# Kernel tuning notes

Measured on AMD Instinct MI355X. Metric: run time of the kernel, lower is better.

The kernel has to match this reference:

```python
import jax, jax.numpy as jnp
import numpy as np

D_MODEL = 768
N_HEAD = 12
HEAD_DIM = D_MODEL // N_HEAD
D_FF = 4 * D_MODEL
EPS = 1e-5


def setup_inputs() -> dict:
    key = jax.random.key(0)
    ks = jax.random.split(key, 12)
    B, S = 4, 1024
    s = 0.02
    return {
        "x": jax.random.normal(ks[0], (B, S, D_MODEL), jnp.float32),
        "ln1_g": jnp.ones((D_MODEL,), jnp.float32),
        "ln1_b": jnp.zeros((D_MODEL,), jnp.float32),
        "ln2_g": jnp.ones((D_MODEL,), jnp.float32),
        "ln2_b": jnp.zeros((D_MODEL,), jnp.float32),
        "w_attn": jax.random.normal(ks[1], (D_MODEL, 3 * D_MODEL), jnp.float32) * s,
        "b_attn": jnp.zeros((3 * D_MODEL,), jnp.float32),
        "w_proj": jax.random.normal(ks[2], (D_MODEL, D_MODEL), jnp.float32) * s,
        "b_proj": jnp.zeros((D_MODEL,), jnp.float32),
        "w_fc": jax.random.normal(ks[3], (D_MODEL, D_FF), jnp.float32) * s,
        "b_fc": jnp.zeros((D_FF,), jnp.float32),
        "w_mlp_proj": jax.random.normal(ks[4], (D_FF, D_MODEL), jnp.float32) * s,
        "b_mlp_proj": jnpp.zeros((D_MODEL,), jnp.float32) if False else jnp.zeros((D_MODEL,), jnp.float32),
    }


def layer_norm(x, g, b):
    mu = jnp.mean(x, axis=-1, keepdims=True)
    var = jnp.mean(jnp.square(x - mu), axis=-1, keepdims=True)
    return (x - mu) * jax.lax.rsqrt(var + EPS) * g + b


def attention(x, w_attn, b_attn, w_proj, b_proj):
    B, S, _ = x.shape
    qkv = x @ w_attn + b_attn                      # [B,S,3D]
    q, k, v = jnp.split(qkv, 3, axis=-1)
    def heads(t):
        return t.reshape(B, S, N_HEAD, HEAD_DIM).transpose(0, 2, 1, 3)  # [B,H,S,hd]
    q, k, v = heads(q), heads(k), heads(v)
    scale = HEAD_DIM ** (-0.5)
    att = jnp.einsum("bhqd,bhkd->bhqk", q, k) * scale
    # additive causal mask: strictly-upper triangle gets -1e9 (matches TF source)
    mask = 1.0 - jnp.tril(jnp.ones((S, S), att.dtype))
    att = att + mask * (-1e9)
    att = jax.nn.softmax(att, axis=-1)
    y = jnp.einsum("bhqk,bhkd->bhqd", att, v)
    y = y.transpose(0, 2, 1, 3).reshape(B, S, D_MODEL)
    return y @ w_proj + b_proj


def mlp(x, w_fc, b_fc, w_mlp_proj, b_mlp_proj):
    h = jax.nn.gelu(x @ w_fc + b_fc, approximate=True)
    return h @ w_mlp_proj + b_mlp_proj


def reference(x, ln1_g, ln1_b, ln2_g, ln2_b, w_attn, b_attn, w_proj, b_proj,
              w_fc, b_fc, w_mlp_proj, b_mlp_proj):
    x = x + attention(layer_norm(x, ln1_g, ln1_b), w_attn, b_attn, w_proj, b_proj)
    x = x + mlp(layer_norm(x, ln2_g, ln2_b), w_fc, b_fc, w_mlp_proj, b_mlp_proj)
    return x
```

## Files before the change

kernel.cpp:

```cpp
#include <hip/hip_runtime.h>

typedef unsigned short u16;
typedef short bf8_t __attribute__((ext_vector_type(8)));
typedef float f32x4 __attribute__((ext_vector_type(4)));

__device__ __forceinline__ u16 f2bf(float f) {
  unsigned u = __builtin_bit_cast(unsigned, f);
  unsigned r = (u + 0x7fffu + ((u >> 16) & 1u)) >> 16;
  return (u16)r;
}

__device__ __forceinline__ void gld16(const void* g, void* l) {
  __builtin_amdgcn_global_load_lds((const __attribute__((address_space(1))) unsigned int*)g,
                                   (__attribute__((address_space(3))) unsigned int*)l, 16, 0, 0);
}

#define MFMA(a, b, c) __builtin_amdgcn_mfma_f32_16x16x32_bf16((a), (b), (c), 0, 0, 0)

__global__ void wtrans_kernel(const float* __restrict__ W, u16* __restrict__ WT, int K, int N) {
  __shared__ float tile[32][33];
  const int n0 = blockIdx.x << 5, k0 = blockIdx.y << 5;
  const int tx = threadIdx.x, ty = threadIdx.y;
#pragma unroll
  for (int i = 0; i < 4; i++) {
    const int r = ty + (i << 3);
    tile[r][tx] = W[(size_t)(k0 + r) * N + n0 + tx];
  }
  __syncthreads();
#pragma unroll
  for (int i = 0; i < 4; i++) {
    const int r = ty + (i << 3);
    WT[(size_t)(n0 + r) * K + k0 + tx] = f2bf(tile[tx][r]);
  }
}

__global__ void ln_kernel(const float* __restrict__ x, const float* __restrict__ g,
                          const float* __restrict__ bb, u16* __restrict__ o) {
  const int row = blockIdx.x, t = threadIdx.x;
  const float* xr = x + (size_t)row * 768;
  float v[3];
#pragma unroll
  for (int i = 0; i < 3; i++) v[i] = xr[t + (i << 8)];
  float s = v[0] + v[1] + v[2];
#pragma unroll
  for (int off = 1; off < 64; off <<= 1) s += __shfl_xor(s, off, 64);
  __shared__ float red[4];
  const int w = t >> 6;
  if ((t & 63) == 0) red[w] = s;
  __syncthreads();
  const float mu = (red[0] + red[1] + red[2] + red[3]) * (1.f / 768.f);
  float q = 0.f;
#pragma unroll
  for (int i = 0; i < 3; i++) {
    v[i] -= mu;
    q += v[i] * v[i];
  }
#pragma unroll
  for (int off = 1; off < 64; off <<= 1) q += __shfl_xor(q, off, 64);
  __syncthreads();
  if ((t & 63) == 0) red[w] = q;
  __syncthreads();
  const float var = (red[0] + red[1] + red[2] + red[3]) * (1.f / 768.f);
  const float rs = rsqrtf(var + 1e-5f);
#pragma unroll
  for (int i = 0; i < 3; i++) {
    const int idx = t + (i << 8);
    o[(size_t)row * 768 + idx] = f2bf(v[i] * rs * g[idx] + bb[idx]);
  }
}

template <int EPI>
__global__ void gemm_kernel(const u16* __restrict__ A, const u16* __restrict__ BT,
                            const float* __restrict__ bias, const float* __restrict__ res,
                            void* __restrict__ outp, int M, int N, int K) {
  __shared__ __align__(16) u16 As[128 * 32];
  __shared__ __align__(16) u16 Bs[128 * 32];
  const int m0 = blockIdx.y << 7, n0 = blockIdx.x << 7;
  const int tid = threadIdx.x, lane = tid & 63, w = tid >> 6;
  const int wr = w >> 1, wc = w & 1;
  const int l16 = lane & 15, kg = lane >> 4;
  f32x4 acc[4][4];
  const f32x4 fz = {0.f, 0.f, 0.f, 0.f};
#pragma unroll
  for (int i = 0; i < 4; i++)
#pragma unroll
    for (int j = 0; j < 4; j++) acc[i][j] = fz;

  const int c1 = (w << 6) + lane;
  const int r1 = c1 >> 2, ko1 = (c1 & 3) << 3;
  const int c2 = c1 + 256;
  const int r2 = c2 >> 2, ko2 = (c2 & 3) << 3;
  const int nkt = K >> 5;
  for (int kt = 0; kt < nkt; kt++) {
    const int k0 = kt << 5;
    __syncthreads();
    gld16(A + (size_t)(m0 + r1) * K + k0 + ko1, As + (size_t)(c1 - lane) * 8);
    gld16(A + (size_t)(m0 + r2) * K + k0 + ko2, As + (size_t)(c2 - lane) * 8);
    gld16(BT + (size_t)(n0 + r1) * K + k0 + ko1, Bs + (size_t)(c1 - lane) * 8);
    gld16(BT + (size_t)(n0 + r2) * K + k0 + ko2, Bs + (size_t)(c2 - lane) * 8);
    __syncthreads();
    bf8_t af[4], bfr[4];
#pragma unroll
    for (int mf = 0; mf < 4; mf++)
      af[mf] = *(const bf8_t*)&As[((wr << 6) + (mf << 4) + l16) * 32 + (kg << 3)];
#pragma unroll
    for (int nf = 0; nf < 4; nf++)
      bfr[nf] = *(const bf8_t*)&Bs[((wc << 6) + (nf << 4) + l16) * 32 + (kg << 3)];
#pragma unroll
    for (int mf = 0; mf < 4; mf++)
#pragma unroll
      for (int nf = 0; nf < 4; nf++) acc[mf][nf] = MFMA(af[mf], bfr[nf], acc[mf][nf]);
  }
#pragma unroll
  for (int mf = 0; mf < 4; mf++) {
#pragma unroll
    for (int nf = 0; nf < 4; nf++) {
      const int col = n0 + (wc << 6) + (nf << 4) + l16;
      const float bv = bias[col];
#pragma unroll
      for (int j = 0; j < 4; j++) {
        const int row = m0 + (wr << 6) + (mf << 4) + (kg << 2) + j;
        float v = acc[mf][nf][j] + bv;
        if constexpr (EPI == 0) {
          ((u16*)outp)[(size_t)row * N + col] = f2bf(v);
        } else if constexpr (EPI == 1) {
          const float u = 0.7978845608f * (v + 0.044715f * v * v * v);
          const float e = __expf(2.f * u);
          const float th = 1.f - 2.f / (e + 1.f);
          ((u16*)outp)[(size_t)row * N + col] = f2bf(0.5f * v * (1.f + th));
        } else {
          v += res[(size_t)row * N + col];
          ((float*)outp)[(size_t)row * N + col] = v;
        }
      }
    }
  }
}

__global__ void attn_kernel(const u16* __restrict__ qkv, u16* __restrict__ y) {
  __shared__ __align__(16) u16 Qs[64 * 64];
  __shared__ __align__(16) u16 Ks[64 * 64];
  __shared__ __align__(16) u16 Vt[64 * 72];
  __shared__ __align__(16) u16 Ps[4][16 * 72];
  const int qt = blockIdx.x, bh = blockIdx.y;
  const int b = bh / 12, h = bh - b * 12;
  const size_t brow = (size_t)b << 10;
  const int q0 = qt << 6;
  const int tid = threadIdx.x, lane = tid & 63, w = tid >> 6;
  const int l16 = lane & 15, kg = lane >> 4;

  const int c1 = (w << 6) + lane, c2 = c1 + 256;
  const int row1 = c1 >> 3, cc1 = c1 & 7;
  const int row2 = c2 >> 3, cc2 = c2 & 7;
  const int sw1 = ((cc1 ^ (row1 & 7)) << 3);
  const int sw2 = ((cc2 ^ (row2 & 7)) << 3);

  {
    const int cb = h << 6;
    gld16(qkv + (brow + q0 + row1) * 2304 + cb + sw1, Qs + (size_t)(c1 - lane) * 8);
    gld16(qkv + (brow + q0 + row2) * 2304 + cb + sw2, Qs + (size_t)(c2 - lane) * 8);
  }
  __syncthreads();
  bf8_t qf[2];
  {
    const int qrow = (w << 4) + l16;
#pragma unroll
    for (int hd = 0; hd < 2; hd++) {
      const int ch = (kg + (hd << 2)) ^ (qrow & 7);
      qf[hd] = *(const bf8_t*)&Qs[qrow * 64 + (ch << 3)];
    }
  }

  f32x4 oacc[4];
  const f32x4 fz = {0.f, 0.f, 0.f, 0.f};
#pragma unroll
  for (int dg = 0; dg < 4; dg++) oacc[dg] = fz;
  float mrun[4], lrun[4];
#pragma unroll
  for (int j = 0; j < 4; j++) {
    mrun[j] = -1e30f;
    lrun[j] = 0.f;
  }

  for (int kt = 0; kt <= qt; kt++) {
    __syncthreads();
    {
      const int cb = 768 + (h << 6);
      gld16(qkv + (brow + (kt << 6) + row1) * 2304 + cb + sw1, Ks + (size_t)(c1 - lane) * 8);
      gld16(qkv + (brow + (kt << 6) + row2) * 2304 + cb + sw2, Ks + (size_t)(c2 - lane) * 8);
    }
    {
      const int cb = 1536 + (h << 6);
#pragma unroll
      for (int ii = 0; ii < 2; ii++) {
        const int c = tid + (ii << 8);
        const int key = c >> 3, d0 = (c & 7) << 3;
        const bf8_t vv = *(const bf8_t*)(qkv + (brow + (kt << 6) + key) * 2304 + cb + d0);
#pragma unroll
        for (int i = 0; i < 8; i++) Vt[(d0 + i) * 72 + key] = (u16)vv[i];
      }
    }
    __syncthreads();
    float sv[4][4];
#pragma unroll
    for (int g = 0; g < 4; g++) {
      f32x4 z = fz;
      const int key = (g << 4) + l16;
#pragma unroll
      for (int hd = 0; hd < 2; hd++) {
        const int ch = (kg + (hd << 2)) ^ (key & 7);
        const bf8_t kf = *(const bf8_t*)&Ks[key * 64 + (ch << 3)];
        z = MFMA(qf[hd], kf, z);
      }
      const int gkey = (kt << 6) + key;
#pragma unroll
      for (int j = 0; j < 4; j++) {
        const int grow = q0 + (w << 4) + (kg << 2) + j;
        sv[g][j] = (gkey <= grow) ? z[j] * 0.125f : -1e30f;
      }
    }
    float tm[4];
#pragma unroll
    for (int j = 0; j < 4; j++)
      tm[j] = fmaxf(fmaxf(sv[0][j], sv[1][j]), fmaxf(sv[2][j], sv[3][j]));
#pragma unroll
    for (int o = 1; o < 16; o <<= 1)
#pragma unroll
      for (int j = 0; j < 4; j++) tm[j] = fmaxf(tm[j], __shfl_xor(tm[j], o, 64));
    float corr[4], tsum[4];
#pragma unroll
    for (int j = 0; j < 4; j++) {
      const float mn = fmaxf(mrun[j], tm[j]);
      corr[j] = __expf(mrun[j] - mn);
      mrun[j] = mn;
      tsum[j] = 0.f;
    }
#pragma unroll
    for (int g = 0; g < 4; g++)
#pragma unroll
      for (int j = 0; j < 4; j++) {
        const float p = __expf(sv[g][j] - mrun[j]);
        sv[g][j] = p;
        tsum[j] += p;
      }
#pragma unroll
    for (int o = 1; o < 16; o <<= 1)
#pragma unroll
      for (int j = 0; j < 4; j++) tsum[j] += __shfl_xor(tsum[j], o, 64);
#pragma unroll
    for (int j = 0; j < 4; j++) lrun[j] = lrun[j] * corr[j] + tsum[j];
#pragma unroll
    for (int dg = 0; dg < 4; dg++)
#pragma unroll
      for (int j = 0; j < 4; j++) oacc[dg][j] *= corr[j];
#pragma unroll
    for (int g = 0; g < 4; g++)
#pragma unroll
      for (int j = 0; j < 4; j++)
        Ps[w][((kg << 2) + j) * 72 + (g << 4) + l16] = f2bf(sv[g][j]);
    bf8_t pf[2];
#pragma unroll
    for (int kh = 0; kh < 2; kh++)
      pf[kh] = *(const bf8_t*)&Ps[w][l16 * 72 + (kg << 3) + (kh << 5)];
#pragma unroll
    for (int dg = 0; dg < 4; dg++)
#pragma unroll
      for (int kh = 0; kh < 2; kh++) {
        const bf8_t vf = *(const bf8_t*)&Vt[((dg << 4) + l16) * 72 + (kg << 3) + (kh << 5)];
        oacc[dg] = MFMA(pf[kh], vf, oacc[dg]);
      }
  }
  float inv[4];
#pragma unroll
  for (int j = 0; j < 4; j++) inv[j] = 1.f / lrun[j];
#pragma unroll
  for (int dg = 0; dg < 4; dg++)
#pragma unroll
    for (int j = 0; j < 4; j++) {
      const size_t grow = brow + q0 + (w << 4) + (kg << 2) + j;
      y[grow * 768 + (h << 6) + (dg << 4) + l16] = f2bf(oacc[dg][j] * inv[j]);
    }
}

extern "C" void kernel_launch(void* const* d_in, const int* in_sizes, int n_in,
                              void* d_out, int out_size, void* d_ws, size_t ws_size,
                              hipStream_t stream) {
  const float* x = (const float*)d_in[0];
  const float* ln1_g = (const float*)d_in[1];
  const float* ln1_b = (const float*)d_in[2];
  const float* ln2_g = (const float*)d_in[3];
  const float* ln2_b = (const float*)d_in[4];
  const float* w_attn = (const float*)d_in[5];
  const float* b_attn = (const float*)d_in[6];
  const float* w_proj = (const float*)d_in[7];
  const float* b_proj = (const float*)d_in[8];
  const float* w_fc = (const float*)d_in[9];
  const float* b_fc = (const float*)d_in[10];
  const float* w_mlp = (const float*)d_in[11];
  const float* b_mlp = (const float*)d_in[12];
  float* out = (float*)d_out;

  char* ws = (char*)d_ws;
  u16* wqkvT = (u16*)(ws + 0);
  u16* wprojT = (u16*)(ws + 3538944);
  u16* wfcT = (u16*)(ws + 4718592);
  u16* wmlpT = (u16*)(ws + 9437184);
  u16* xn = (u16*)(ws + 14155776);
  u16* qkv = (u16*)(ws + 20447232);
  u16* hbuf = (u16*)(ws + 20447232);
  u16* yb = (u16*)(ws + 45613056);
  float* x1 = (float*)(ws + 51904512);

  const dim3 wtb(32, 8);
  wtrans_kernel<<<dim3(2304 / 32, 768 / 32), wtb, 0, stream>>>(w_attn, wqkvT, 768, 2304);
  wtrans_kernel<<<dim3(768 / 32, 768 / 32), wtb, 0, stream>>>(w_proj, wprojT, 768, 768);
  wtrans_kernel<<<dim3(3072 / 32, 768 / 32), wtb, 0, stream>>>(w_fc, wfcT, 768, 3072);
  wtrans_kernel<<<dim3(768 / 32, 3072 / 32), wtb, 0, stream>>>(w_mlp, wmlpT, 3072, 768);

  ln_kernel<<<4096, 256, 0, stream>>>(x, ln1_g, ln1_b, xn);
  gemm_kernel<0><<<dim3(2304 / 128, 4096 / 128), 256, 0, stream>>>(xn, wqkvT, b_attn, nullptr,
                                                                   qkv, 4096, 2304, 768);
  attn_kernel<<<dim3(16, 48), 256, 0, stream>>>(qkv, yb);
  gemm_kernel<2><<<dim3(768 / 128, 4096 / 128), 256, 0, stream>>>(yb, wprojT, b_proj, x, x1,
                                                                  4096, 768, 768);
  ln_kernel<<<4096, 256, 0, stream>>>(x1, ln2_g, ln2_b, xn);
  gemm_kernel<1><<<dim3(3072 / 128, 4096 / 128), 256, 0, stream>>>(xn, wfcT, b_fc, nullptr,
                                                                   hbuf, 4096, 3072, 768);
  gemm_kernel<2><<<dim3(768 / 128, 4096 / 128), 256, 0, stream>>>(hbuf, wmlpT, b_mlp, x1, out,
                                                                  4096, 768, 3072);
}
```

Measured before the change: 246.4 us.

## Double-buffer K/V tiles, prefetch next tile, swizzle V^T, reverse q-tile order

The attention kernel now double-buffers the K and transposed-V shared-memory tiles. The next K tile is issued via async global-to-LDS loads and the next V tile is loaded into registers while the current tile is being computed, which removes one barrier per iteration and hides global load latency. The V^T layout drops its padding in favour of an XOR swizzle to avoid LDS bank conflicts. Query tiles are launched in reverse order so the longest causal blocks start first, which helps load balance, at the cost of more LDS use and register pressure.

Result: faster. 229.5 us (-6.9%).

```diff
diff --git a/kernel.cpp b/kernel.cpp
--- a/kernel.cpp
+++ b/kernel.cpp
@@ -139,38 +139,37 @@
 
 __global__ void attn_kernel(const u16* __restrict__ qkv, u16* __restrict__ y) {
   __shared__ __align__(16) u16 Qs[64 * 64];
-  __shared__ __align__(16) u16 Ks[64 * 64];
-  __shared__ __align__(16) u16 Vt[64 * 72];
+  __shared__ __align__(16) u16 Ks[2][64 * 64];
+  __shared__ __align__(16) u16 Vt[2][64 * 64];
   __shared__ __align__(16) u16 Ps[4][16 * 72];
-  const int qt = blockIdx.x, bh = blockIdx.y;
+  const int qt = (int)gridDim.x - 1 - (int)blockIdx.x;
+  const int bh = blockIdx.y;
   const int b = bh / 12, h = bh - b * 12;
   const size_t brow = (size_t)b << 10;
   const int q0 = qt << 6;
   const int tid = threadIdx.x, lane = tid & 63, w = tid >> 6;
   const int l16 = lane & 15, kg = lane >> 4;
 
-  const int c1 = (w << 6) + lane, c2 = c1 + 256;
+  const int c1 = tid, c2 = tid + 256;
   const int row1 = c1 >> 3, cc1 = c1 & 7;
   const int row2 = c2 >> 3, cc2 = c2 & 7;
   const int sw1 = ((cc1 ^ (row1 & 7)) << 3);
   const int sw2 = ((cc2 ^ (row2 & 7)) << 3);
-
-  {
-    const int cb = h << 6;
-    gld16(qkv + (brow + q0 + row1) * 2304 + cb + sw1, Qs + (size_t)(c1 - lane) * 8);
-    gld16(qkv + (brow + q0 + row2) * 2304 + cb + sw2, Qs + (size_t)(c2 - lane) * 8);
-  }
-  __syncthreads();
+  const int sg1 = ((cc1 & 1) << 2) | (cc1 & 2) | ((cc1 >> 2) & 1);
+  const int sg2 = ((cc2 & 1) << 2) | (cc2 & 2) | ((cc2 >> 2) & 1);
+  const int vcol1 = row1 ^ (sg1 << 3), d01 = cc1 << 3;
+  const int vcol2 = row2 ^ (sg2 << 3), d02 = cc2 << 3;
+
+  const int cbQ = h << 6, cbK = 768 + (h << 6), cbV = 1536 + (h << 6);
+
+  gld16(qkv + (brow + q0 + row1) * 2304 + cbQ + sw1, Qs + (size_t)(c1 - lane) * 8);
+  gld16(qkv + (brow + q0 + row2) * 2304 + cbQ + sw2, Qs + (size_t)(c2 - lane) * 8);
+  gld16(qkv + (brow + row1) * 2304 + cbK + sw1, Ks[0] + (size_t)(c1 - lane) * 8);
+  gld16(qkv + (brow + row2) * 2304 + cbK + sw2, Ks[0] + (size_t)(c2 - lane) * 8);
+  bf8_t v1 = *(const bf8_t*)(qkv + (brow + row1) * 2304 + cbV + (cc1 << 3));
+  bf8_t v2 = *(const bf8_t*)(qkv + (brow + row2) * 2304 + cbV + (cc2 << 3));
+
   bf8_t qf[2];
-  {
-    const int qrow = (w << 4) + l16;
-#pragma unroll
-    for (int hd = 0; hd < 2; hd++) {
-      const int ch = (kg + (hd << 2)) ^ (qrow & 7);
-      qf[hd] = *(const bf8_t*)&Qs[qrow * 64 + (ch << 3)];
-    }
-  }
-
   f32x4 oacc[4];
   const f32x4 fz = {0.f, 0.f, 0.f, 0.f};
 #pragma unroll
@@ -183,24 +182,31 @@
   }
 
   for (int kt = 0; kt <= qt; kt++) {
+    const int cur = kt & 1;
+    u16* Vc = Vt[cur];
+#pragma unroll
+    for (int i = 0; i < 8; i++) Vc[(d01 + i) * 64 + vcol1] = (u16)v1[i];
+#pragma unroll
+    for (int i = 0; i < 8; i++) Vc[(d02 + i) * 64 + vcol2] = (u16)v2[i];
     __syncthreads();
-    {
-      const int cb = 768 + (h << 6);
-      gld16(qkv + (brow + (kt << 6) + row1) * 2304 + cb + sw1, Ks + (size_t)(c1 - lane) * 8);
-      gld16(qkv + (brow + (kt << 6) + row2) * 2304 + cb + sw2, Ks + (size_t)(c2 - lane) * 8);
-    }
-    {
-      const int cb = 1536 + (h << 6);
-#pragma unroll
-      for (int ii = 0; ii < 2; ii++) {
-        const int c = tid + (ii << 8);
-        const int key = c >> 3, d0 = (c & 7) << 3;
-        const bf8_t vv = *(const bf8_t*)(qkv + (brow + (kt << 6) + key) * 2304 + cb + d0);
-#pragma unroll
-        for (int i = 0; i < 8; i++) Vt[(d0 + i) * 72 + key] = (u16)vv[i];
-      }
-    }
-    __syncthreads();
+
+    if (kt == 0) {
+      const int qrow = (w << 4) + l16;
+#pragma unroll
+      for (int hd = 0; hd < 2; hd++) {
+        const int ch = (kg + (hd << 2)) ^ (qrow & 7);
+        qf[hd] = *(const bf8_t*)&Qs[qrow * 64 + (ch << 3)];
+      }
+    }
+    if (kt < qt) {
+      const int nr = (kt + 1) << 6;
+      gld16(qkv + (brow + nr + row1) * 2304 + cbK + sw1, Ks[cur ^ 1] + (size_t)(c1 - lane) * 8);
+      gld16(qkv + (brow + nr + row2) * 2304 + cbK + sw2, Ks[cur ^ 1] + (size_t)(c2 - lane) * 8);
+      v1 = *(const bf8_t*)(qkv + (brow + nr + row1) * 2304 + cbV + (cc1 << 3));
+      v2 = *(const bf8_t*)(qkv + (brow + nr + row2) * 2304 + cbV + (cc2 << 3));
+    }
+
+    const u16* Kc = Ks[cur];
     float sv[4][4];
 #pragma unroll
     for (int g = 0; g < 4; g++) {
@@ -209,7 +215,7 @@
 #pragma unroll
       for (int hd = 0; hd < 2; hd++) {
         const int ch = (kg + (hd << 2)) ^ (key & 7);
-        const bf8_t kf = *(const bf8_t*)&Ks[key * 64 + (ch << 3)];
+        const bf8_t kf = *(const bf8_t*)&Kc[key * 64 + (ch << 3)];
         z = MFMA(qf[hd], kf, z);
       }
       const int gkey = (kt << 6) + key;
@@ -263,12 +269,15 @@
     for (int kh = 0; kh < 2; kh++)
       pf[kh] = *(const bf8_t*)&Ps[w][l16 * 72 + (kg << 3) + (kh << 5)];
 #pragma unroll
-    for (int dg = 0; dg < 4; dg++)
+    for (int dg = 0; dg < 4; dg++) {
+      const int sgr = (((l16 >> 3) & 1) << 2) | ((dg & 1) << 1) | (dg >> 1);
+      const int d = (dg << 4) + l16;
 #pragma unroll
       for (int kh = 0; kh < 2; kh++) {
-        const bf8_t vf = *(const bf8_t*)&Vt[((dg << 4) + l16) * 72 + (kg << 3) + (kh << 5)];
+        const bf8_t vf = *(const bf8_t*)&Vc[d * 64 + ((((kh << 2) + kg) ^ sgr) << 3)];
         oacc[dg] = MFMA(pf[kh], vf, oacc[dg]);
       }
+    }
   }
   float inv[4];
 #pragma unroll
```
